# Performance work log

Measured on AMD Instinct MI355X. Metric: run time of the kernel, lower is better.

## Reference

```python
import jax, jax.numpy as jnp
import numpy as np

T = 3              # num_ntype (slots)
NH = 64            # num_hidden == num_classes
HEADS = (4, 4, 1)
NUM_ETYPES = 5
EDGE_DIM = 64
N_NODES = 20000
NEG_SLOPE = 0.2
ALPHA = 0.05       # residual-attention blend
EPS = 1e-12


def _l2_by_slot(x):
    # l2_norm with l2BySlot='True': normalize each ntype slot independently
    n = x.shape[0]
    xs = x.reshape(n, T, -1)
    nrm = jnp.linalg.norm(xs, axis=2, keepdims=True)
    return (xs / jnp.maximum(nrm, EPS)).reshape(n, -1)


def _edge_softmax(logits, dst, n):
    # softmax over incoming edges of each destination node
    m = jax.lax.stop_gradient(jax.ops.segment_max(logits, dst, num_segments=n))
    e = jnp.exp(logits - m[dst])
    s = jax.ops.segment_sum(e, dst, num_segments=n)
    return e / s[dst]


def _conv(x, src, dst, etype, W, al, ar, ee_tab, We, ae, res_attn, act):
    # slotGATConv: x [N,T,C], W [T,C,H*O], al/ar [H,T*O], ee_tab [R,De], We [De,H*De], ae [H,De]
    n = x.shape[0]
    H = al.shape[0]
    proj = jnp.einsum('ntc,tcd->ntd', x, W)                     # [N,T,H*O]
    O = proj.shape[-1] // H
    feat = proj.reshape(n, T, H, O).transpose(0, 2, 1, 3).reshape(n, H, T * O)
    el = jnp.einsum('nhd,hd->nh', feat, al)
    er = jnp.einsum('nhd,hd->nh', feat, ar)
    De = ee_tab.shape[1]
    ep = (ee_tab[etype] @ We).reshape(-1, H, De)                # [E,H,De]
    ee = jnp.einsum('ehd,hd->eh', ep, ae)                       # [E,H]
    logit = jax.nn.leaky_relu(el[src] + er[dst] + ee, NEG_SLOPE)
    a = _edge_softmax(logit, dst, n)                            # [E,H]
    if res_attn is not None:
        a = a * (1.0 - ALPHA) + res_attn * ALPHA
    out = jax.ops.segment_sum(feat[src] * a[:, :, None], dst, num_segments=n)  # [N,H,T*O]
    if act:
        out = jax.nn.elu(out)
    return out, a


def _forward(feat0, feat1, feat2, w_in0, b_in0, w_in1, b_in1, w_in2, b_in2,
             l0_W, l0_al, l0_ar, l0_ee, l0_we, l0_ae,
             l1_W, l1_al, l1_ar, l1_ee, l1_we, l1_ae,
             l2_W, l2_al, l2_ar, l2_ee, l2_we, l2_ae,
             dm_W, e_feat, src, dst, left, right, mid):
    feats = [feat0, feat1, feat2]
    lins = [(w_in0, b_in0), (w_in1, b_in1), (w_in2, b_in2)]
    blocks = []
    for t, (f, (w, b)) in enumerate(zip(feats, lins)):
        ft = f @ w + b                                          # [n_t, NH]
        pad = jnp.zeros((f.shape[0], T * NH), ft.dtype)
        blocks.append(pad.at[:, t * NH:(t + 1) * NH].set(ft))   # slot zero-padding
    h = jnp.concatenate(blocks, 0)                              # [N, T*NH]
    emb = [_l2_by_slot(h)]                                      # aggregator='None' -> identity
    x = h.reshape(-1, T, NH)
    out0, a0 = _conv(x, src, dst, e_feat, l0_W, l0_al, l0_ar, l0_ee, l0_we, l0_ae, None, True)
    emb.append(_l2_by_slot(out0.mean(1)))
    x = out0.reshape(-1, HEADS[0], T, NH).transpose(0, 2, 1, 3).reshape(-1, T, HEADS[0] * NH)
    out1, a1 = _conv(x, src, dst, e_feat, l1_W, l1_al, l1_ar, l1_ee, l1_we, l1_ae, a0, True)
    emb.append(_l2_by_slot(out1.mean(1)))
    x = out1.reshape(-1, HEADS[1], T, NH).transpose(0, 2, 1, 3).reshape(-1, T, HEADS[1] * NH)
    out2, _ = _conv(x, src, dst, e_feat, l2_W, l2_al, l2_ar, l2_ee, l2_we, l2_ae, a1, False)
    emb.append(_l2_by_slot(out2.mean(1)))
    # aggregator='None' + inProcessEmb='True': concat per-slot along feature dim
    embs = [e.reshape(-1, T, NH) for e in emb]
    o = jnp.concatenate(embs, 2).reshape(-1, T * NH * len(embs))  # [N, 768]
    le, re = o[left], o[right]
    scores = jnp.zeros(left.shape[0], o.dtype)
    for r in range(NUM_ETYPES):                                 # DistMult per relation
        s = ((le @ dm_W[r]) * re).sum(1)
        scores = jnp.where(mid == r, s, scores)
    return jax.nn.sigmoid(scores)


def setup_inputs() -> dict:
    key = jax.random.key(0)
    ks = iter(jax.random.split(key, 64))
    def nrm(shape, std):
        return jax.random.normal(next(ks), shape, jnp.float32) * std
    counts = [8000, 6000, 6000]
    in_dims = [256, 128, 64]
    inp = {}
    for t in range(T):
        inp[f'feat{t}'] = jax.random.normal(next(ks), (counts[t], in_dims[t]), jnp.float32)
        inp[f'w_in{t}'] = nrm((in_dims[t], NH), 0.1)
        inp[f'b_in{t}'] = nrm((NH,), 0.1)
    Cs = [NH, HEADS[0] * NH, HEADS[1] * NH]
    for l in range(3):
        H = HEADS[l]
        inp[f'l{l}_W'] = nrm((T, Cs[l], H * NH), 0.1)
        inp[f'l{l}_al'] = nrm((H, T * NH), 0.1)
        inp[f'l{l}_ar'] = nrm((H, T * NH), 0.1)
        inp[f'l{l}_ee'] = nrm((NUM_ETYPES, EDGE_DIM), 0.1)
        inp[f'l{l}_we'] = nrm((EDGE_DIM, H * EDGE_DIM), 0.1)
        inp[f'l{l}_ae'] = nrm((H, EDGE_DIM), 0.1)
    D = T * NH * 4
    inp['dm_W'] = nrm((NUM_ETYPES, D, D), 0.05)
    E, L = 200000, 10000
    inp['e_feat'] = jax.random.randint(next(ks), (E,), 0, NUM_ETYPES)
    inp['src'] = jax.random.randint(next(ks), (E,), 0, N_NODES)
    inp['dst'] = jax.random.randint(next(ks), (E,), 0, N_NODES)
    inp['left'] = jax.random.randint(next(ks), (L,), 0, N_NODES)
    inp['right'] = jax.random.randint(next(ks), (L,), 0, N_NODES)
    inp['mid'] = jax.random.randint(next(ks), (L,), 0, NUM_ETYPES)
    return inp


def reference(feat0, feat1, feat2, w_in0, b_in0, w_in1, b_in1, w_in2, b_in2,
              l0_W, l0_al, l0_ar, l0_ee, l0_we, l0_ae,
              l1_W, l1_al, l1_ar, l1_ee, l1_we, l1_ae,
              l2_W, l2_al, l2_ar, l2_ee, l2_we, l2_ae,
              dm_W, e_feat, src, dst, left, right, mid):
    return _forward(feat0, feat1, feat2, w_in0, b_in0, w_in1, b_in1, w_in2, b_in2,
                    l0_W, l0_al, l0_ar, l0_ee, l0_we, l0_ae,
                    l1_W, l1_al, l1_ar, l1_ee, l1_we, l1_ae,
                    l2_W, l2_al, l2_ar, l2_ee, l2_we, l2_ae,
                    dm_W, e_feat, src, dst, left, right, mid)
```

## Files before the change

### kernel.cpp

```cpp
#include <hip/hip_runtime.h>
#include <math.h>

#define N_NODES 20000
#define NPAD    20096
#define N_EDGES 200000
#define N_PAIRS 10000
#define PAIR_PAD 10368
#define DM_TILES 162
#define NBLK    79

typedef __attribute__((ext_vector_type(8))) short s16x8;
typedef __attribute__((ext_vector_type(4))) float f32x4;

__device__ inline float wave_max(float v){
  for (int o = 32; o > 0; o >>= 1) v = fmaxf(v, __shfl_xor(v, o));
  return v;
}
__device__ inline float wave_sum(float v){
  for (int o = 32; o > 0; o >>= 1) v += __shfl_xor(v, o);
  return v;
}
__device__ inline short f2bf(float x){
  union { float f; unsigned u; } v; v.f = x;
  unsigned r = (v.u + 0x7FFFu + ((v.u >> 16) & 1u)) >> 16;
  return (short)r;
}
__device__ inline float bf2f(short s){
  union { unsigned u; float f; } v; v.u = ((unsigned)(unsigned short)s) << 16;
  return v.f;
}
__device__ inline int ntype(int s){ return (s < 8000) ? 0 : ((s < 14000) ? 1 : 2); }

__global__ void build_h(const float* __restrict__ f0, const float* __restrict__ w0, const float* __restrict__ b0,
                        const float* __restrict__ f1, const float* __restrict__ w1, const float* __restrict__ b1,
                        const float* __restrict__ f2, const float* __restrict__ w2, const float* __restrict__ b2,
                        short* __restrict__ Xb0, short* __restrict__ o_b,
                        int* __restrict__ cnt3, int* __restrict__ cnt5, int* __restrict__ pos5,
                        float* __restrict__ score, int* __restrict__ pairs,
                        float* __restrict__ eall, short* __restrict__ Xb12,
                        short* __restrict__ featb){
  const int blk = blockIdx.x, lane = threadIdx.x;
  const int gid = blk * 64 + lane;
  if (gid < 80000) cnt3[gid] = 0;
  if (gid < 5){ cnt5[gid * 16] = 0; pos5[gid * 16] = 0; }
  if (gid < 10016) score[gid] = 0.f;
  if (gid < PAIR_PAD) pairs[gid] = -1;
  for (int i = gid; i < 480000; i += 160000) eall[i] = 0.f;
  s16x8 z = {};
  if (gid < 4608){
    int t = (gid * 16) / 24576, off = (gid * 16) % 24576;
    short* p = Xb12 + ((size_t)(t * NPAD + N_NODES)) * 256 + off;
    *(s16x8*)p = z; *(s16x8*)(p + 8) = z;
  }
  if (gid < 1152){
    int t = (gid * 16) / 6144, off = (gid * 16) % 6144;
    short* p = Xb0 + ((size_t)(t * NPAD + N_NODES)) * 64 + off;
    *(s16x8*)p = z; *(s16x8*)(p + 8) = z;
  }
  int t, C, nbase; const float *f, *w, *b;
  if (blk < 1000)       { t = 0; nbase = 0;     C = 256; f = f0; w = w0; b = b0; }
  else if (blk < 1750)  { t = 1; nbase = 8000;  C = 128; f = f1; w = w1; b = b1; }
  else                  { t = 2; nbase = 14000; C = 64;  f = f2; w = w2; b = b2; }
  const int n0 = blk * 8;
  const int n0l = n0 - nbase;
  __shared__ float xs[8 * 256];
  const float* fr = f + (size_t)n0l * C;
  for (int i = lane; i < 8 * C; i += 64) xs[i] = fr[i];
  __syncthreads();
  float acc[8];
#pragma unroll
  for (int j = 0; j < 8; j++) acc[j] = b[lane];
  for (int c = 0; c < C; c++){
    float wv = w[c * 64 + lane];
#pragma unroll
    for (int j = 0; j < 8; j++) acc[j] += xs[j * C + c] * wv;
  }
  for (int j = 0; j < 8; j++){
    int n = n0 + j;
    {
      int h = lane >> 4, si = (lane >> 3) & 1, j8 = lane & 7;
      int s0 = (t == 0) ? 1 : 0;
      int s1 = (t == 2) ? 1 : 2;
      int toff = si ? s1 : s0;
      *(s16x8*)(featb + ((size_t)n * 4 + h) * 192 + toff * 64 + j8 * 8) = z;
    }
    for (int tt = 0; tt < 3; tt++)
      Xb0[((size_t)(tt * NPAD) + n) * 64 + lane] = f2bf((tt == t) ? acc[j] : 0.f);
    float ss = wave_sum(acc[j] * acc[j]);
    float sc = 1.f / fmaxf(sqrtf(ss), 1e-12f);
    for (int tt = 0; tt < 3; tt++)
      o_b[(size_t)n * 768 + tt * 256 + lane] = f2bf((tt == t) ? acc[j] * sc : 0.f);
  }
}

__global__ void count_prep_k(const int* __restrict__ dst, const int* __restrict__ srcv,
                             int* __restrict__ cnt3,
                             const int* __restrict__ mid, int* __restrict__ cnt5,
                             const float* __restrict__ lW0, const float* __restrict__ lW1,
                             const float* __restrict__ lW2, const float* __restrict__ dmW,
                             short* __restrict__ Wt0, short* __restrict__ Wt1,
                             short* __restrict__ Wt2, short* __restrict__ Mt,
                             const float* __restrict__ ee0, const float* __restrict__ we0, const float* __restrict__ ae0,
                             const float* __restrict__ ee1, const float* __restrict__ we1, const float* __restrict__ ae1,
                             const float* __restrict__ ee2, const float* __restrict__ we2, const float* __restrict__ ae2,
                             float* __restrict__ ee5f){
  if (blockIdx.x < 782){
    int e = blockIdx.x * 256 + threadIdx.x;
    int lane = threadIdx.x & 63;
    if (e < N_EDGES){
      int tt = ntype(srcv[e]);
      atomicAdd(&cnt3[dst[e] * 4 + tt], 1);
    }
    int r_mine = (e < N_PAIRS) ? mid[e] : -1;
#pragma unroll
    for (int r = 0; r < 5; r++){
      unsigned long long mask = __ballot(r_mine == r);
      if (mask){
        int leader = __ffsll((long long)mask) - 1;
        if (lane == leader) atomicAdd(&cnt5[r * 16], __popcll(mask));
      }
    }
    return;
  }
  int lin = blockIdx.x - 782;
  int z = lin / 576;
  int rem = lin % 576;
  int by = rem / 24, bx = rem % 24;
  if (z == 10){
    int r = bx, L = by;
    if (r >= 5 || L >= 3) return;
    int H = (L == 2) ? 1 : 4;
    const float* eetab = (L == 0) ? ee0 : ((L == 1) ? ee1 : ee2);
    const float* We    = (L == 0) ? we0 : ((L == 1) ? we1 : we2);
    const float* ae    = (L == 0) ? ae0 : ((L == 1) ? ae1 : ae2);
    int h = threadIdx.x >> 6, lane = threadIdx.x & 63;
    if (h >= H) return;
    float v = 0.f;
    for (int k = 0; k < 64; k++) v += eetab[r * 64 + k] * We[k * H * 64 + h * 64 + lane];
    v *= ae[h * 64 + lane];
    v = wave_sum(v);
    if (lane == 0) ee5f[L * 32 + r * H + h] = v;
    return;
  }
  const float* s; short* d; int R, Cc, r0, c0;
  if (z < 5){
    s = dmW + (size_t)z * 589824; d = Mt + (size_t)z * 589824;
    R = 768; Cc = 768; r0 = bx * 32; c0 = by * 32;
  } else if (z < 8){
    if (bx >= 8 || by >= 8) return;
    int t = z - 5;
    s = lW1 + (size_t)t * 65536; d = Wt1 + (size_t)t * 65536;
    R = 256; Cc = 256; r0 = bx * 32; c0 = by * 32;
  } else if (z == 8){
    if (bx >= 6 || by >= 8) return;
    int t = bx >> 1;
    s = lW0 + (size_t)t * 16384; d = Wt0 + (size_t)t * 16384;
    R = 64; Cc = 256; r0 = (bx & 1) * 32; c0 = by * 32;
  } else {
    if (bx >= 8 || by >= 6) return;
    int t = by >> 1;
    s = lW2 + (size_t)t * 16384; d = Wt2 + (size_t)t * 16384;
    R = 256; Cc = 64; r0 = bx * 32; c0 = (by & 1) * 32;
  }
  __shared__ float tile[32][33];
  int tx = threadIdx.x & 31, ty = threadIdx.x >> 5;
  for (int i = 0; i < 32; i += 8){
    int r = r0 + ty + i;
    tile[ty + i][tx] = (r < R && c0 + tx < Cc) ? s[(size_t)r * Cc + c0 + tx] : 0.f;
  }
  __syncthreads();
  for (int i = 0; i < 32; i += 8){
    int c = c0 + ty + i;
    if (c < Cc && r0 + tx < R)
      d[(size_t)c * R + r0 + tx] = f2bf(tile[tx][ty + i]);
  }
}

__global__ void scan1_k(const int* __restrict__ cnt3, int* __restrict__ loc, int* __restrict__ bsum){
  __shared__ int s[256];
  int tid = threadIdx.x;
  int idx = blockIdx.x * 256 + tid;
  int v = (idx < N_NODES) ? (cnt3[idx * 4] + cnt3[idx * 4 + 1] + cnt3[idx * 4 + 2]) : 0;
  s[tid] = v;
  __syncthreads();
  for (int o = 1; o < 256; o <<= 1){
    int u = (tid >= o) ? s[tid - o] : 0;
    __syncthreads();
    s[tid] += u;
    __syncthreads();
  }
  if (idx < N_NODES) loc[idx] = s[tid] - v;
  if (tid == 255) bsum[blockIdx.x] = s[255];
}

__global__ void scan2_k(const int* __restrict__ bsum, int* __restrict__ bofs,
                        const int* __restrict__ cnt5, int* __restrict__ off5){
  __shared__ int s[128];
  int tid = threadIdx.x;
  int v = (tid < NBLK) ? bsum[tid] : 0;
  s[tid] = v;
  __syncthreads();
  for (int o = 1; o < 128; o <<= 1){
    int u = (tid >= o) ? s[tid - o] : 0;
    __syncthreads();
    s[tid] += u;
    __syncthreads();
  }
  if (tid < NBLK) bofs[tid] = s[tid] - v;
  if (tid == 0){
    int r0 = 0;
    for (int r = 0; r < 5; r++){ off5[r] = r0; r0 += ((cnt5[r * 16] + 63) >> 6) << 6; }
  }
}

__global__ void scan3_k(const int* __restrict__ loc, const int* __restrict__ bofs,
                        int* __restrict__ coff, int* __restrict__ cpos,
                        const int* __restrict__ cnt3){
  int idx = blockIdx.x * 256 + threadIdx.x;
  if (idx < N_NODES){
    int v = loc[idx] + bofs[blockIdx.x];
    coff[idx] = v;
    int c0 = cnt3[idx * 4], c1 = cnt3[idx * 4 + 1];
    cpos[idx * 4]     = v;
    cpos[idx * 4 + 1] = v + c0;
    cpos[idx * 4 + 2] = v + c0 + c1;
  }
  if (idx == 0) coff[N_NODES] = N_EDGES;
}

__global__ void scatter_k(const int* __restrict__ dst, const int* __restrict__ srcv,
                          const int* __restrict__ efeat, int* __restrict__ cpos,
                          int* __restrict__ src_sorted, int* __restrict__ et_sorted,
                          const int* __restrict__ mid, const int* __restrict__ off5,
                          int* __restrict__ pos5, int* __restrict__ pairs){
  int e = blockIdx.x * 256 + threadIdx.x;
  int lane = threadIdx.x & 63;
  if (e < N_EDGES){
    int s = srcv[e];
    int tt = ntype(s);
    int p = atomicAdd(&cpos[dst[e] * 4 + tt], 1);
    src_sorted[p] = s;
    et_sorted[p] = efeat[e];
  }
  int r_mine = (e < N_PAIRS) ? mid[e] : -1;
#pragma unroll
  for (int r = 0; r < 5; r++){
    unsigned long long mask = __ballot(r_mine == r);
    if (mask){
      int cnt = __popcll(mask);
      int leader = __ffsll((long long)mask) - 1;
      int base = 0;
      if (lane == leader) base = atomicAdd(&pos5[r * 16], cnt);
      base = __shfl(base, leader);
      if (r_mine == r){
        int rank = __popcll(mask & ((1ull << lane) - 1ull));
        pairs[off5[r] + base + rank] = e;
      }
    }
  }
}

template<int C, int NO, int TYPED>
__global__ void mfma_proj(const short* __restrict__ Xb, const short* __restrict__ Wt,
                          short* __restrict__ featb, const float* __restrict__ al,
                          const float* __restrict__ ar, float* __restrict__ elf,
                          float* __restrict__ erf){
  constexpr int H = NO / 64;
  const int ct = blockIdx.y;
  const int t  = blockIdx.z;
  int tile = blockIdx.x;
  if (TYPED){
    const int lo[3] = {0, 62, 109};
    const int hi[3] = {63, 110, 157};
    tile += lo[t];
    if (tile >= hi[t]) return;
  }
  const int n0 = tile * 128;
  const int tid = threadIdx.x;
  const int w = tid >> 6, lane = tid & 63;
  const int quad = lane >> 4, ln = lane & 15;
  __shared__ __attribute__((aligned(16))) short A_s[128 * 32];
  __shared__ __attribute__((aligned(16))) short B_s[64 * 32];
  const short* Xt  = Xb + (size_t)t * NPAD * C;
  const short* Wtt = Wt + ((size_t)t * NO + ct * 64) * C;
  f32x4 acc[2][4] = {};
  for (int kk = 0; kk < C; kk += 32){
    {
      int row = tid >> 1, half = tid & 1;
      const s16x8* g = (const s16x8*)(Xt + (size_t)(n0 + row) * C + kk + half * 16);
      s16x8 v0 = g[0], v1 = g[1];
      *(s16x8*)(A_s + row * 32 + half * 16) = v0;
      *(s16x8*)(A_s + row * 32 + half * 16 + 8) = v1;
    }
    {
      int row = tid >> 2, chunk = tid & 3;
      s16x8 v = *(const s16x8*)(Wtt + (size_t)row * C + kk + chunk * 8);
      *(s16x8*)(B_s + row * 32 + chunk * 8) = v;
    }
    __syncthreads();
    s16x8 af0 = *(s16x8*)(A_s + (w * 32 + ln) * 32 + quad * 8);
    s16x8 af1 = *(s16x8*)(A_s + (w * 32 + 16 + ln) * 32 + quad * 8);
    s16x8 bf[4];
#pragma unroll
    for (int b = 0; b < 4; b++) bf[b] = *(s16x8*)(B_s + (b * 16 + ln) * 32 + quad * 8);
#pragma unroll
    for (int b = 0; b < 4; b++){
      acc[0][b] = __builtin_amdgcn_mfma_f32_16x16x32_bf16(af0, bf[b], acc[0][b], 0, 0, 0);
      acc[1][b] = __builtin_amdgcn_mfma_f32_16x16x32_bf16(af1, bf[b], acc[1][b], 0, 0, 0);
    }
    __syncthreads();
  }
#pragma unroll
  for (int ar_ = 0; ar_ < 2; ar_++){
#pragma unroll
    for (int i = 0; i < 4; i++){
      int n = n0 + w * 32 + ar_ * 16 + quad * 4 + i;
      if (n >= N_NODES) continue;
#pragma unroll
      for (int b = 0; b < 4; b++){
        int jj = b * 16 + ln;
        featb[((size_t)n * H + ct) * 192 + t * 64 + jj] = f2bf(acc[ar_][b][i]);
      }
    }
  }
  float alv[4], arv[4];
#pragma unroll
  for (int b = 0; b < 4; b++){
    alv[b] = al[ct * 192 + t * 64 + b * 16 + ln];
    arv[b] = ar[ct * 192 + t * 64 + b * 16 + ln];
  }
#pragma unroll
  for (int ar_ = 0; ar_ < 2; ar_++){
#pragma unroll
    for (int i = 0; i < 4; i++){
      float pe = 0.f, pr = 0.f;
#pragma unroll
      for (int b = 0; b < 4; b++){
        pe += acc[ar_][b][i] * alv[b];
        pr += acc[ar_][b][i] * arv[b];
      }
#pragma unroll
      for (int o = 1; o < 16; o <<= 1){
        pe += __shfl_xor(pe, o);
        pr += __shfl_xor(pr, o);
      }
      int n = n0 + w * 32 + ar_ * 16 + quad * 4 + i;
      if (ln == 0 && n < N_NODES){
        atomicAdd(&elf[n * H + ct], pe);
        atomicAdd(&erf[n * H + ct], pr);
      }
    }
  }
}

template<int H, int MODE, int ACT, int TYPED>
__global__ __launch_bounds__(256) void gat_fused(
    const int* __restrict__ csr_off, const int* __restrict__ src_sorted,
    const int* __restrict__ et_sorted,
    const float* __restrict__ el, const float* __restrict__ er, const float* __restrict__ ee5,
    const float* __restrict__ aprev, float* __restrict__ aout,
    const short* __restrict__ featb, short* __restrict__ outb,
    short* __restrict__ o_b, const int* __restrict__ cnt3, int kslice){
  const int wid = threadIdx.x >> 6, lane = threadIdx.x & 63;
  const int n = blockIdx.x * 4 + wid;
  if (n >= N_NODES) return;
  const int off = csr_off[n];
  const int cnt = csr_off[n + 1] - off;
  __shared__ float a_s[4][64][H];
  __shared__ int   src_s[4][64];
  __shared__ float out_s[4][H * 192];
  float ern[H];
#pragma unroll
  for (int h = 0; h < H; h++) ern[h] = er[n * H + h];

  if (cnt <= 64){
    int p = off + lane;
    int sidx = 0, r = 0;
    if (lane < cnt){ sidx = src_sorted[p]; r = et_sorted[p]; }
    int src0 = (cnt > 0) ? src_sorted[off] : 0;
    src_s[wid][lane] = (lane < cnt) ? sidx : src0;
    float lg[H];
#pragma unroll
    for (int h = 0; h < H; h++) lg[h] = -1e30f;
    if (lane < cnt){
#pragma unroll
      for (int h = 0; h < H; h++){
        float v = el[sidx * H + h] + ern[h] + ee5[r * H + h];
        lg[h] = (v >= 0.f) ? v : 0.2f * v;
      }
    }
    float ap[4] = {};
    if (MODE > 0 && lane < cnt){
#pragma unroll
      for (int q = 0; q < 4; q++) ap[q] = aprev[(size_t)p * 4 + q];
    }
    float av[H];
#pragma unroll
    for (int h = 0; h < H; h++){
      float mh = wave_max(lg[h]);
      float ex = (lane < cnt) ? __expf(lg[h] - mh) : 0.f;
      float sh = wave_sum(ex);
      float a = ex / sh;
      if (MODE == 1) a = 0.95f * a + 0.05f * ap[h];
      if (MODE == 2) a = 0.95f * a + 0.0125f * (ap[0] + ap[1] + ap[2] + ap[3]);
      av[h] = a;
      a_s[wid][lane][h] = (lane < cnt) ? a : 0.f;
    }
    if constexpr (MODE != 2){
      if (lane < cnt){
        f32x4 o = {av[0], av[1], av[2], av[3]};
        *(f32x4*)(aout + (size_t)p * 4) = o;
      }
    }

    if constexpr (TYPED && H == 4){
      const int q = lane & 31, eo = lane >> 5;
      const int hh = q >> 3, j8 = q & 7;
      float acc[3][8] = {};
      const int b1 = cnt3[n * 4], b2 = b1 + cnt3[n * 4 + 1];
      const int rb[4] = {0, b1, b2, cnt};
#pragma unroll
      for (int t = 0; t < 3; t++){
        for (int b = rb[t]; b < rb[t + 1]; b += 2){
          int e = b + eo;
          bool vld = e < rb[t + 1];
          int ei = vld ? e : rb[t + 1] - 1;
          int s = src_s[wid][ei];
          float a = vld ? a_s[wid][ei][hh] : 0.f;
          s16x8 fv = *(const s16x8*)(featb + ((size_t)s * 4 + hh) * 192 + t * 64 + j8 * 8);
#pragma unroll
          for (int i = 0; i < 8; i++) acc[t][i] += a * bf2f(fv[i]);
        }
      }
#pragma unroll
      for (int t = 0; t < 3; t++){
#pragma unroll
        for (int i = 0; i < 8; i++){
          float tot = acc[t][i] + __shfl_xor(acc[t][i], 32);
          if (lane < 32) out_s[wid][(hh * 24 + t * 8 + j8) * 8 + i] = tot;
        }
      }
    } else if constexpr (H == 4){
      const int p0 = lane;
      const int p1 = (lane < 32) ? lane + 64 : lane - 32;
      const int p2 = lane + 32;
      const int hA = p0 / 24, hB = p1 / 24, hC = p2 / 24;
      float acc0[8] = {}, acc1[8] = {}, acc2[8] = {};
      const int cnt2 = (cnt + 1) & ~1;
      for (int b = 0; b < cnt2; b += 2){
        int eB = b + (lane >> 5), eC = b + 1;
        int sA = src_s[wid][b], sB = src_s[wid][eB], sC = src_s[wid][eC];
        float aA = a_s[wid][b][hA];
        float aB = a_s[wid][eB][hB];
        float aC = a_s[wid][eC][hC];
        s16x8 fA = *(const s16x8*)(featb + (size_t)sA * 768 + p0 * 8);
        s16x8 fB = *(const s16x8*)(featb + (size_t)sB * 768 + p1 * 8);
        s16x8 fC = *(const s16x8*)(featb + (size_t)sC * 768 + p2 * 8);
#pragma unroll
        for (int i = 0; i < 8; i++){
          acc0[i] += aA * bf2f(fA[i]);
          acc1[i] += aB * bf2f(fB[i]);
          acc2[i] += aC * bf2f(fC[i]);
        }
      }
#pragma unroll
      for (int i = 0; i < 8; i++){
        float v1 = (lane < 32) ? acc2[i] : acc1[i];
        float r1 = __shfl_xor(v1, 32);
        out_s[wid][p0 * 8 + i] = acc0[i] + r1;
        float r2 = __shfl_xor(acc2[i], 32);
        if (lane < 32) out_s[wid][p1 * 8 + i] = acc1[i] + r2;
      }
    } else {
      const int eo = lane & 7, cb = lane >> 3;
      float acc[3][8] = {};
      for (int b = 0; b < cnt; b += 8){
        int e = b + eo;
        float a = a_s[wid][e][0];
        int s = src_s[wid][e];
#pragma unroll
        for (int c = 0; c < 3; c++){
          s16x8 fv = *(const s16x8*)(featb + (size_t)s * 192 + (cb * 3 + c) * 8);
#pragma unroll
          for (int i = 0; i < 8; i++) acc[c][i] += a * bf2f(fv[i]);
        }
      }
#pragma unroll
      for (int c = 0; c < 3; c++){
#pragma unroll
        for (int i = 0; i < 8; i++){
          float v = acc[c][i];
          v += __shfl_xor(v, 1); v += __shfl_xor(v, 2); v += __shfl_xor(v, 4);
          if (eo == 0) out_s[wid][(cb * 3 + c) * 8 + i] = v;
        }
      }
    }
  } else {
    constexpr int NC = H * 192 / 8;
    const int c0 = lane, h0 = (c0 / 24) % H;
    const int c1 = lane + 64, h1 = (c1 / 24) % H;
    const bool act0 = (c0 < NC);
    const bool act1 = (H == 4) && (lane < 32);
    float acc0[8] = {}, acc1[8] = {};
    float mh[H], sh[H];
#pragma unroll
    for (int h = 0; h < H; h++){ mh[h] = -1e30f; sh[h] = 0.f; }
    for (int b = lane; b < cnt; b += 64){
      int p = off + b; int s = src_sorted[p]; int r = et_sorted[p];
#pragma unroll
      for (int h = 0; h < H; h++){
        float v = el[s * H + h] + ern[h] + ee5[r * H + h];
        v = (v >= 0.f) ? v : 0.2f * v;
        mh[h] = fmaxf(mh[h], v);
      }
    }
#pragma unroll
    for (int h = 0; h < H; h++) mh[h] = wave_max(mh[h]);
    for (int b = lane; b < cnt; b += 64){
      int p = off + b; int s = src_sorted[p]; int r = et_sorted[p];
#pragma unroll
      for (int h = 0; h < H; h++){
        float v = el[s * H + h] + ern[h] + ee5[r * H + h];
        v = (v >= 0.f) ? v : 0.2f * v;
        sh[h] += __expf(v - mh[h]);
      }
    }
#pragma unroll
    for (int h = 0; h < H; h++) sh[h] = wave_sum(sh[h]);
    if (MODE != 2){
      for (int b = lane; b < cnt; b += 64){
        int p = off + b; int s = src_sorted[p]; int r = et_sorted[p];
        float ap[4] = {};
        if (MODE > 0){
#pragma unroll
          for (int q = 0; q < 4; q++) ap[q] = aprev[(size_t)p * 4 + q];
        }
        float av[4] = {};
#pragma unroll
        for (int h = 0; h < H; h++){
          float v = el[s * H + h] + ern[h] + ee5[r * H + h];
          v = (v >= 0.f) ? v : 0.2f * v;
          float a = __expf(v - mh[h]) / sh[h];
          if (MODE == 1) a = 0.95f * a + 0.05f * ap[h];
          av[h] = a;
        }
        f32x4 o = {av[0], av[1], av[2], av[3]};
        *(f32x4*)(aout + (size_t)p * 4) = o;
      }
    }
    for (int b = 0; b < cnt; b++){
      int p = off + b; int s = src_sorted[p]; int r = et_sorted[p];
      const short* row = featb + (size_t)s * (H * 192);
      float apm[4] = {};
      if (MODE > 0){
#pragma unroll
        for (int q = 0; q < 4; q++) apm[q] = aprev[(size_t)p * 4 + q];
      }
      if (act0){
        float v = el[s * H + h0] + ern[h0] + ee5[r * H + h0];
        v = (v >= 0.f) ? v : 0.2f * v;
        float a = __expf(v - mh[h0]) / sh[h0];
        if (MODE == 1) a = 0.95f * a + 0.05f * apm[h0];
        if (MODE == 2) a = 0.95f * a + 0.0125f * (apm[0] + apm[1] + apm[2] + apm[3]);
        s16x8 vv = *(const s16x8*)(row + c0 * 8);
#pragma unroll
        for (int i = 0; i < 8; i++) acc0[i] += a * bf2f(vv[i]);
      }
      if (act1){
        float v = el[s * H + h1] + ern[h1] + ee5[r * H + h1];
        v = (v >= 0.f) ? v : 0.2f * v;
        float a = __expf(v - mh[h1]) / sh[h1];
        if (MODE == 1) a = 0.95f * a + 0.05f * apm[h1];
        s16x8 vv = *(const s16x8*)(row + c1 * 8);
#pragma unroll
        for (int i = 0; i < 8; i++) acc1[i] += a * bf2f(vv[i]);
      }
    }
    if (act0){
#pragma unroll
      for (int i = 0; i < 8; i++) out_s[wid][c0 * 8 + i] = acc0[i];
    }
    if (act1){
#pragma unroll
      for (int i = 0; i < 8; i++) out_s[wid][c1 * 8 + i] = acc1[i];
    }
  }

  constexpr int NC = H * 192 / 8;
  {
    const int c0 = lane;
    if (c0 < NC){
      float v[8];
#pragma unroll
      for (int i = 0; i < 8; i++) v[i] = out_s[wid][c0 * 8 + i];
      if (ACT){
#pragma unroll
        for (int i = 0; i < 8; i++) v[i] = (v[i] > 0.f) ? v[i] : expm1f(v[i]);
      }
      if (outb){
        int dd = c0 * 8, h = dd / 192, rr = dd % 192, t = rr / 64, j = rr % 64;
        s16x8 o;
#pragma unroll
        for (int i = 0; i < 8; i++) o[i] = f2bf(v[i]);
        *(s16x8*)(outb + ((size_t)(t * NPAD) + n) * 256 + h * 64 + j) = o;
      }
      if (ACT){
#pragma unroll
        for (int i = 0; i < 8; i++) out_s[wid][c0 * 8 + i] = v[i];
      }
    }
    if constexpr (H == 4){
      if (lane < 32){
        const int c1 = lane + 64;
        float v[8];
#pragma unroll
        for (int i = 0; i < 8; i++) v[i] = out_s[wid][c1 * 8 + i];
        if (ACT){
#pragma unroll
          for (int i = 0; i < 8; i++) v[i] = (v[i] > 0.f) ? v[i] : expm1f(v[i]);
        }
        if (outb){
          int dd = c1 * 8, h = dd / 192, rr = dd % 192, t = rr / 64, j = rr % 64;
          s16x8 o;
#pragma unroll
          for (int i = 0; i < 8; i++) o[i] = f2bf(v[i]);
          *(s16x8*)(outb + ((size_t)(t * NPAD) + n) * 256 + h * 64 + j) = o;
        }
        if (ACT){
#pragma unroll
          for (int i = 0; i < 8; i++) out_s[wid][c1 * 8 + i] = v[i];
        }
      }
    }
  }
  for (int t = 0; t < 3; t++){
    float v;
    if (H == 4)
      v = 0.25f * (out_s[wid][t * 64 + lane] + out_s[wid][192 + t * 64 + lane] +
                   out_s[wid][384 + t * 64 + lane] + out_s[wid][576 + t * 64 + lane]);
    else
      v = out_s[wid][t * 64 + lane];
    float ss = wave_sum(v * v);
    float sc = 1.f / fmaxf(sqrtf(ss), 1e-12f);
    o_b[(size_t)n * 768 + t * 256 + kslice * 64 + lane] = f2bf(v * sc);
  }
}

__global__ void distmult_mfma(const short* __restrict__ o_b, const short* __restrict__ Mt,
                              const int* __restrict__ pairs, const int* __restrict__ left,
                              const int* __restrict__ right, const int* __restrict__ mid,
                              float* __restrict__ score){
  const int pt = blockIdx.x, ct = blockIdx.y;
  const int tid = threadIdx.x;
  const int w = tid >> 6, lane = tid & 63;
  const int quad = lane >> 4, ln = lane & 15;
  __shared__ __attribute__((aligned(16))) short smem[8192];
  short* A_s = smem;
  short* B_s = smem + 2048;
  __shared__ int pid_s[64];
  __shared__ int lbase[64];
  if (tid < 64){
    int p = pairs[pt * 64 + tid];
    pid_s[tid] = p;
    lbase[tid] = (p >= 0) ? left[p] * 768 : 0;
  }
  __syncthreads();
  int p0 = pid_s[0];
  if (p0 < 0) return;
  const int r = mid[p0];
  const short* Mr = Mt + (size_t)r * 768 * 768;
  f32x4 acc[8] = {};
  for (int kk = 0; kk < 768; kk += 32){
    {
      int row = tid >> 2, chunk = tid & 3;
      s16x8 v = *(const s16x8*)(o_b + (size_t)lbase[row] + kk + chunk * 8);
      *(s16x8*)(A_s + row * 32 + chunk * 8) = v;
    }
    {
      int row = tid >> 1, half = tid & 1;
      const s16x8* g = (const s16x8*)(Mr + (size_t)(ct * 128 + row) * 768 + kk + half * 16);
      s16x8 v0 = g[0], v1 = g[1];
      *(s16x8*)(B_s + row * 32 + half * 16) = v0;
      *(s16x8*)(B_s + row * 32 + half * 16 + 8) = v1;
    }
    __syncthreads();
    s16x8 af = *(s16x8*)(A_s + (w * 16 + ln) * 32 + quad * 8);
#pragma unroll
    for (int b = 0; b < 8; b++){
      s16x8 bf = *(s16x8*)(B_s + (b * 16 + ln) * 32 + quad * 8);
      acc[b] = __builtin_amdgcn_mfma_f32_16x16x32_bf16(af, bf, acc[b], 0, 0, 0);
    }
    __syncthreads();
  }
  short* RE_s = smem;
  {
    int row = tid >> 2, quarter = tid & 3;
    int p = pid_s[row];
    s16x8 v0 = {}, v1 = {}, v2 = {}, v3 = {};
    if (p >= 0){
      const s16x8* g = (const s16x8*)(o_b + (size_t)right[p] * 768 + ct * 128 + quarter * 32);
      v0 = g[0]; v1 = g[1]; v2 = g[2]; v3 = g[3];
    }
    __syncthreads();
    short* dst = RE_s + row * 128 + quarter * 32;
    *(s16x8*)(dst)      = v0;
    *(s16x8*)(dst + 8)  = v1;
    *(s16x8*)(dst + 16) = v2;
    *(s16x8*)(dst + 24) = v3;
  }
  __syncthreads();
#pragma unroll
  for (int i = 0; i < 4; i++){
    int row = w * 16 + quad * 4 + i;
    float s = 0.f;
#pragma unroll
    for (int b = 0; b < 8; b++)
      s += acc[b][i] * bf2f(RE_s[row * 128 + b * 16 + ln]);
    s += __shfl_xor(s, 1); s += __shfl_xor(s, 2);
    s += __shfl_xor(s, 4); s += __shfl_xor(s, 8);
    if (ln == 0){
      int p = pid_s[row];
      if (p >= 0) atomicAdd(&score[p], s);
    }
  }
}

__global__ void sigmoid_k(const float* __restrict__ score, float* __restrict__ out){
  int i = blockIdx.x * 256 + threadIdx.x;
  if (i < N_PAIRS) out[i] = 1.f / (1.f + __expf(-score[i]));
}

extern "C" void kernel_launch(void* const* d_in, const int* in_sizes, int n_in,
                              void* d_out, int out_size, void* d_ws, size_t ws_size,
                              hipStream_t stream){
  const float* f0 = (const float*)d_in[0];
  const float* w0 = (const float*)d_in[1];
  const float* b0 = (const float*)d_in[2];
  const float* f1 = (const float*)d_in[3];
  const float* w1 = (const float*)d_in[4];
  const float* b1 = (const float*)d_in[5];
  const float* f2 = (const float*)d_in[6];
  const float* w2_ = (const float*)d_in[7];
  const float* b2 = (const float*)d_in[8];
  const float* lW[3]  = {(const float*)d_in[9],  (const float*)d_in[15], (const float*)d_in[21]};
  const float* lal[3] = {(const float*)d_in[10], (const float*)d_in[16], (const float*)d_in[22]};
  const float* lar[3] = {(const float*)d_in[11], (const float*)d_in[17], (const float*)d_in[23]};
  const float* lee[3] = {(const float*)d_in[12], (const float*)d_in[18], (const float*)d_in[24]};
  const float* lwe[3] = {(const float*)d_in[13], (const float*)d_in[19], (const float*)d_in[25]};
  const float* lae[3] = {(const float*)d_in[14], (const float*)d_in[20], (const float*)d_in[26]};
  const float* dmW = (const float*)d_in[27];
  const int* efeat = (const int*)d_in[28];
  const int* srcv  = (const int*)d_in[29];
  const int* dstv  = (const int*)d_in[30];
  const int* left  = (const int*)d_in[31];
  const int* right = (const int*)d_in[32];
  const int* midv  = (const int*)d_in[33];
  float* out = (float*)d_out;

  short* feat_b = (short*)d_ws;
  float* aA     = (float*)(feat_b + 15360000);
  float* aB     = aA + 800000;
  float* eall   = aB + 800000;
  float* ee5f   = eall + 480000;
  float* score  = ee5f + 96;
  int* cnt3     = (int*)(score + 10016);
  int* csr_off  = cnt3 + 80000;
  int* csr_pos  = csr_off + 20004;
  int* loc      = csr_pos + 80000;
  int* bsum     = loc + 20000;
  int* bofs     = bsum + 128;
  int* src_sorted = bofs + 128;
  int* et_sorted  = src_sorted + 200000;
  int* cnt5     = et_sorted + 200000;
  int* off5     = cnt5 + 80;
  int* pos5     = off5 + 8;
  int* pairs    = pos5 + 80;
  short* o_b    = (short*)(pairs + PAIR_PAD);
  short* Xb0    = o_b + 15360000;
  short* Xb12   = Xb0 + 3858432;
  short* Wt0    = Xb12 + 15433728;
  short* Wt1    = Wt0 + 49152;
  short* Wt2    = Wt1 + 196608;
  short* Mt     = Wt2 + 49152;
  float* elf0 = eall, *erf0 = eall + 80000;
  float* elf1 = eall + 160000, *erf1 = eall + 240000;
  float* elf2 = eall + 320000, *erf2 = eall + 400000;

  build_h<<<2500, 64, 0, stream>>>(f0, w0, b0, f1, w1, b1, f2, w2_, b2, Xb0, o_b,
                                   cnt3, cnt5, pos5, score, pairs, eall, Xb12, feat_b);
  count_prep_k<<<782 + 6336, 256, 0, stream>>>(dstv, srcv, cnt3, midv, cnt5,
                                               lW[0], lW[1], lW[2], dmW, Wt0, Wt1, Wt2, Mt,
                                               lee[0], lwe[0], lae[0], lee[1], lwe[1], lae[1],
                                               lee[2], lwe[2], lae[2], ee5f);
  scan1_k<<<NBLK, 256, 0, stream>>>(cnt3, loc, bsum);
  scan2_k<<<1, 128, 0, stream>>>(bsum, bofs, cnt5, off5);
  scan3_k<<<NBLK, 256, 0, stream>>>(loc, bofs, csr_off, csr_pos, cnt3);
  scatter_k<<<782, 256, 0, stream>>>(dstv, srcv, efeat, csr_pos, src_sorted, et_sorted,
                                     midv, off5, pos5, pairs);

  { dim3 g(64, 4, 3);
    mfma_proj<64, 256, 1><<<g, 256, 0, stream>>>(Xb0, Wt0, feat_b, lal[0], lar[0], elf0, erf0); }
  gat_fused<4, 0, 1, 1><<<5000, 256, 0, stream>>>(csr_off, src_sorted, et_sorted, elf0, erf0, ee5f,
                                                  nullptr, aA, feat_b, Xb12, o_b, cnt3, 1);

  { dim3 g(NPAD / 128, 4, 3);
    mfma_proj<256, 256, 0><<<g, 256, 0, stream>>>(Xb12, Wt1, feat_b, lal[1], lar[1], elf1, erf1); }
  gat_fused<4, 1, 1, 0><<<5000, 256, 0, stream>>>(csr_off, src_sorted, et_sorted, elf1, erf1, ee5f + 32,
                                                  aA, aB, feat_b, Xb12, o_b, cnt3, 2);

  { dim3 g(NPAD / 128, 1, 3);
    mfma_proj<256, 64, 0><<<g, 256, 0, stream>>>(Xb12, Wt2, feat_b, lal[2], lar[2], elf2, erf2); }
  gat_fused<1, 2, 0, 0><<<5000, 256, 0, stream>>>(csr_off, src_sorted, et_sorted, elf2, erf2, ee5f + 64,
                                                  aB, nullptr, feat_b, nullptr, o_b, cnt3, 3);

  { dim3 g(DM_TILES, 6); distmult_mfma<<<g, 256, 0, stream>>>(o_b, Mt, pairs, left, right, midv, score); }
  sigmoid_k<<<40, 256, 0, stream>>>(score, out);
}
```

Baseline: 469.9 us.

## Transpose out_s smem layout, vectorize loads, fold ELU, and unroll gather loop by four

Changes the shared-memory output buffer to a padded transposed layout (stride 100) so that per-lane 8-element writes and reads avoid LDS bank conflicts. ELU is now applied in registers before the store, which removes an extra shared-memory read-modify-write pass. Source offsets are pre-scaled into byte offsets, el/er/ee5/aprev are read with vector loads, and the H=4 untyped gather is unrolled to handle four edges per iteration so more loads are in flight. The changes trade higher register pressure for less address arithmetic and fewer memory instructions.

```diff
diff --git a/kernel.cpp b/kernel.cpp
--- a/kernel.cpp
+++ b/kernel.cpp
@@ -30,6 +30,9 @@
   return v.f;
 }
 __device__ inline int ntype(int s){ return (s < 8000) ? 0 : ((s < 14000) ? 1 : 2); }
+__device__ inline float elu1(float x){ return (x > 0.f) ? x : expm1f(x); }
+
+#define OS(i, c) ((i) * 100 + (c))
 
 __global__ void build_h(const float* __restrict__ f0, const float* __restrict__ w0, const float* __restrict__ b0,
                         const float* __restrict__ f1, const float* __restrict__ w1, const float* __restrict__ b1,
@@ -368,31 +371,44 @@
   const int cnt = csr_off[n + 1] - off;
   __shared__ float a_s[4][64][H];
   __shared__ int   src_s[4][64];
-  __shared__ float out_s[4][H * 192];
+  __shared__ float out_s[4][800];
   float ern[H];
-#pragma unroll
-  for (int h = 0; h < H; h++) ern[h] = er[n * H + h];
+  if constexpr (H == 4){
+    f32x4 ev = *(const f32x4*)(er + n * 4);
+#pragma unroll
+    for (int h = 0; h < 4; h++) ern[h] = ev[h];
+  } else {
+    ern[0] = er[n];
+  }
 
   if (cnt <= 64){
     int p = off + lane;
     int sidx = 0, r = 0;
     if (lane < cnt){ sidx = src_sorted[p]; r = et_sorted[p]; }
-    int src0 = (cnt > 0) ? src_sorted[off] : 0;
-    src_s[wid][lane] = (lane < cnt) ? sidx : src0;
+    int src0 = __shfl(sidx, 0);
+    src_s[wid][lane] = ((lane < cnt) ? sidx : src0) * (H * 384);
     float lg[H];
 #pragma unroll
     for (int h = 0; h < H; h++) lg[h] = -1e30f;
     if (lane < cnt){
-#pragma unroll
-      for (int h = 0; h < H; h++){
-        float v = el[sidx * H + h] + ern[h] + ee5[r * H + h];
-        lg[h] = (v >= 0.f) ? v : 0.2f * v;
+      if constexpr (H == 4){
+        f32x4 elv = *(const f32x4*)(el + sidx * 4);
+        f32x4 eev = *(const f32x4*)(ee5 + r * 4);
+#pragma unroll
+        for (int h = 0; h < 4; h++){
+          float v = elv[h] + ern[h] + eev[h];
+          lg[h] = (v >= 0.f) ? v : 0.2f * v;
+        }
+      } else {
+        float v = el[sidx] + ern[0] + ee5[r];
+        lg[0] = (v >= 0.f) ? v : 0.2f * v;
       }
     }
     float ap[4] = {};
     if (MODE > 0 && lane < cnt){
-#pragma unroll
-      for (int q = 0; q < 4; q++) ap[q] = aprev[(size_t)p * 4 + q];
+      f32x4 av4 = *(const f32x4*)(aprev + (size_t)p * 4);
+#pragma unroll
+      for (int q = 0; q < 4; q++) ap[q] = av4[q];
     }
     float av[H];
 #pragma unroll
@@ -412,6 +428,7 @@
         *(f32x4*)(aout + (size_t)p * 4) = o;
       }
     }
+    const char* fb = (const char*)featb;
 
     if constexpr (TYPED && H == 4){
       const int q = lane & 31, eo = lane >> 5;
@@ -421,13 +438,14 @@
       const int rb[4] = {0, b1, b2, cnt};
 #pragma unroll
       for (int t = 0; t < 3; t++){
+        const int sub = hh * 384 + t * 128 + j8 * 16;
         for (int b = rb[t]; b < rb[t + 1]; b += 2){
           int e = b + eo;
           bool vld = e < rb[t + 1];
           int ei = vld ? e : rb[t + 1] - 1;
-          int s = src_s[wid][ei];
+          int so = src_s[wid][ei];
           float a = vld ? a_s[wid][ei][hh] : 0.f;
-          s16x8 fv = *(const s16x8*)(featb + ((size_t)s * 4 + hh) * 192 + t * 64 + j8 * 8);
+          s16x8 fv = *(const s16x8*)(fb + so + sub);
 #pragma unroll
           for (int i = 0; i < 8; i++) acc[t][i] += a * bf2f(fv[i]);
         }
@@ -437,7 +455,8 @@
 #pragma unroll
         for (int i = 0; i < 8; i++){
           float tot = acc[t][i] + __shfl_xor(acc[t][i], 32);
-          if (lane < 32) out_s[wid][(hh * 24 + t * 8 + j8) * 8 + i] = tot;
+          if (ACT) tot = elu1(tot);
+          if (lane < 32) out_s[wid][OS(i, hh * 24 + t * 8 + j8)] = tot;
         }
       }
     } else if constexpr (H == 4){
@@ -445,31 +464,41 @@
       const int p1 = (lane < 32) ? lane + 64 : lane - 32;
       const int p2 = lane + 32;
       const int hA = p0 / 24, hB = p1 / 24, hC = p2 / 24;
+      const int eo2 = lane >> 5;
       float acc0[8] = {}, acc1[8] = {}, acc2[8] = {};
-      const int cnt2 = (cnt + 1) & ~1;
-      for (int b = 0; b < cnt2; b += 2){
-        int eB = b + (lane >> 5), eC = b + 1;
-        int sA = src_s[wid][b], sB = src_s[wid][eB], sC = src_s[wid][eC];
-        float aA = a_s[wid][b][hA];
-        float aB = a_s[wid][eB][hB];
-        float aC = a_s[wid][eC][hC];
-        s16x8 fA = *(const s16x8*)(featb + (size_t)sA * 768 + p0 * 8);
-        s16x8 fB = *(const s16x8*)(featb + (size_t)sB * 768 + p1 * 8);
-        s16x8 fC = *(const s16x8*)(featb + (size_t)sC * 768 + p2 * 8);
+      const int cnt4 = (cnt + 3) & ~3;
+      for (int b = 0; b < cnt4; b += 4){
+        int eB0 = b + eo2, eB1 = b + 2 + eo2;
+        int oA0 = src_s[wid][b],     oB0 = src_s[wid][eB0], oC0 = src_s[wid][b + 1];
+        int oA1 = src_s[wid][b + 2], oB1 = src_s[wid][eB1], oC1 = src_s[wid][b + 3];
+        float aA0 = a_s[wid][b][hA],     aB0 = a_s[wid][eB0][hB], aC0 = a_s[wid][b + 1][hC];
+        float aA1 = a_s[wid][b + 2][hA], aB1 = a_s[wid][eB1][hB], aC1 = a_s[wid][b + 3][hC];
+        s16x8 fA0 = *(const s16x8*)(fb + oA0 + p0 * 16);
+        s16x8 fB0 = *(const s16x8*)(fb + oB0 + p1 * 16);
+        s16x8 fC0 = *(const s16x8*)(fb + oC0 + p2 * 16);
+        s16x8 fA1 = *(const s16x8*)(fb + oA1 + p0 * 16);
+        s16x8 fB1 = *(const s16x8*)(fb + oB1 + p1 * 16);
+        s16x8 fC1 = *(const s16x8*)(fb + oC1 + p2 * 16);
 #pragma unroll
         for (int i = 0; i < 8; i++){
-          acc0[i] += aA * bf2f(fA[i]);
-          acc1[i] += aB * bf2f(fB[i]);
-          acc2[i] += aC * bf2f(fC[i]);
+          acc0[i] += aA0 * bf2f(fA0[i]) + aA1 * bf2f(fA1[i]);
+          acc1[i] += aB0 * bf2f(fB0[i]) + aB1 * bf2f(fB1[i]);
+          acc2[i] += aC0 * bf2f(fC0[i]) + aC1 * bf2f(fC1[i]);
         }
       }
 #pragma unroll
       for (int i = 0; i < 8; i++){
         float v1 = (lane < 32) ? acc2[i] : acc1[i];
         float r1 = __shfl_xor(v1, 32);
-        out_s[wid][p0 * 8 + i] = acc0[i] + r1;
+        float v0 = acc0[i] + r1;
+        if (ACT) v0 = elu1(v0);
+        out_s[wid][OS(i, p0)] = v0;
         float r2 = __shfl_xor(acc2[i], 32);
-        if (lane < 32) out_s[wid][p1 * 8 + i] = acc1[i] + r2;
+        if (lane < 32){
+          float vv = acc1[i] + r2;
+          if (ACT) vv = elu1(vv);
+          out_s[wid][OS(i, p1)] = vv;
+        }
       }
     } else {
       const int eo = lane & 7, cb = lane >> 3;
@@ -477,10 +506,10 @@
       for (int b = 0; b < cnt; b += 8){
         int e = b + eo;
         float a = a_s[wid][e][0];
-        int s = src_s[wid][e];
+        int so = src_s[wid][e];
 #pragma unroll
         for (int c = 0; c < 3; c++){
-          s16x8 fv = *(const s16x8*)(featb + (size_t)s * 192 + (cb * 3 + c) * 8);
+          s16x8 fv = *(const s16x8*)(fb + so + (cb * 3 + c) * 16);
 #pragma unroll
           for (int i = 0; i < 8; i++) acc[c][i] += a * bf2f(fv[i]);
         }
@@ -491,7 +520,8 @@
         for (int i = 0; i < 8; i++){
           float v = acc[c][i];
           v += __shfl_xor(v, 1); v += __shfl_xor(v, 2); v += __shfl_xor(v, 4);
-          if (eo == 0) out_s[wid][(cb * 3 + c) * 8 + i] = v;
+          if (ACT) v = elu1(v);
+          if (eo == 0) out_s[wid][OS(i, cb * 3 + c)] = v;
         }
       }
     }
@@ -578,68 +608,55 @@
     }
     if (act0){
 #pragma unroll
-      for (int i = 0; i < 8; i++) out_s[wid][c0 * 8 + i] = acc0[i];
+      for (int i = 0; i < 8; i++){
+        float v = ACT ? elu1(acc0[i]) : acc0[i];
+        out_s[wid][OS(i, c0)] = v;
+      }
     }
     if (act1){
 #pragma unroll
-      for (int i = 0; i < 8; i++) out_s[wid][c1 * 8 + i] = acc1[i];
+      for (int i = 0; i < 8; i++){
+        float v = ACT ? elu1(acc1[i]) : acc1[i];
+        out_s[wid][OS(i, c1)] = v;
+      }
     }
   }
 
   constexpr int NC = H * 192 / 8;
-  {
-    const int c0 = lane;
-    if (c0 < NC){
-      float v[8];
-#pragma unroll
-      for (int i = 0; i < 8; i++) v[i] = out_s[wid][c0 * 8 + i];
-      if (ACT){
-#pragma unroll
-        for (int i = 0; i < 8; i++) v[i] = (v[i] > 0.f) ? v[i] : expm1f(v[i]);
-      }
-      if (outb){
+  if (outb){
+    {
+      const int c0 = lane;
+      if (c0 < NC){
         int dd = c0 * 8, h = dd / 192, rr = dd % 192, t = rr / 64, j = rr % 64;
         s16x8 o;
 #pragma unroll
-        for (int i = 0; i < 8; i++) o[i] = f2bf(v[i]);
+        for (int i = 0; i < 8; i++) o[i] = f2bf(out_s[wid][OS(i, c0)]);
         *(s16x8*)(outb + ((size_t)(t * NPAD) + n) * 256 + h * 64 + j) = o;
-      }
-      if (ACT){
-#pragma unroll
-        for (int i = 0; i < 8; i++) out_s[wid][c0 * 8 + i] = v[i];
       }
     }
     if constexpr (H == 4){
       if (lane < 32){
         const int c1 = lane + 64;
-        float v[8];
-#pragma unroll
-        for (int i = 0; i < 8; i++) v[i] = out_s[wid][c1 * 8 + i];
-        if (ACT){
-#pragma unroll
-          for (int i = 0; i < 8; i++) v[i] = (v[i] > 0.f) ? v[i] : expm1f(v[i]);
-        }
-        if (outb){
-          int dd = c1 * 8, h = dd / 192, rr = dd % 192, t = rr / 64, j = rr % 64;
-          s16x8 o;
-#pragma unroll
-          for (int i = 0; i < 8; i++) o[i] = f2bf(v[i]);
-          *(s16x8*)(outb + ((size_t)(t * NPAD) + n) * 256 + h * 64 + j) = o;
-        }
-        if (ACT){
-#pragma unroll
-          for (int i = 0; i < 8; i++) out_s[wid][c1 * 8 + i] = v[i];
-        }
+        int dd = c1 * 8, h = dd / 192, rr = dd % 192, t = rr / 64, j = rr % 64;
+        s16x8 o;
+#pragma unroll
+        for (int i = 0; i < 8; i++) o[i] = f2bf(out_s[wid][OS(i, c1)]);
+        *(s16x8*)(outb + ((size_t)(t * NPAD) + n) * 256 + h * 64 + j) = o;
       }
     }
   }
   for (int t = 0; t < 3; t++){
     float v;
-    if (H == 4)
-      v = 0.25f * (out_s[wid][t * 64 + lane] + out_s[wid][192 + t * 64 + lane] +
-                   out_s[wid][384 + t * 64 + lane] + out_s[wid][576 + t * 64 + lane]);
-    else
-      v = out_s[wid][t * 64 + lane];
+    if (H == 4){
+      int d0 = t * 64 + lane;
+      v = 0.25f * (out_s[wid][OS(d0 & 7, d0 >> 3)] +
+                   out_s[wid][OS(d0 & 7, 24 + (d0 >> 3))] +
+                   out_s[wid][OS(d0 & 7, 48 + (d0 >> 3))] +
+                   out_s[wid][OS(d0 & 7, 72 + (d0 >> 3))]);
+    } else {
+      int d0 = t * 64 + lane;
+      v = out_s[wid][OS(d0 & 7, d0 >> 3)];
+    }
     float ss = wave_sum(v * v);
     float sc = 1.f / fmaxf(sqrtf(ss), 1e-12f);
     o_b[(size_t)n * 768 + t * 256 + kslice * 64 + lane] = f2bf(v * sc);
```

New measurement: 466.5 us. About the same (-0.7%).
